# Kernel tuning notes

Hardware: AMD Instinct MI355X
Metric: run time of the kernel (lower is better)

Reference implementation:

```python
import jax, jax.numpy as jnp
import numpy as np

DIM = 256
QK_DIM = 256
NUM_HEADS = 8
N_WIN = 7
TOPK = 4
SCALE = QK_DIM ** (-0.5)


def setup_inputs() -> dict:
    key = jax.random.key(0)
    k1, k2, k3 = jax.random.split(key, 3)
    N, D, H, W, C = 2, 8, 56, 56, DIM
    x = jax.random.normal(k1, (N, D, H, W, C), dtype=jnp.float32)
    # QKVLinear: Linear(dim, qk_dim + qk_dim + dim)
    Wqkv = jax.random.normal(k2, (C, 2 * QK_DIM + DIM), dtype=jnp.float32) * 0.02
    bqkv = jnp.zeros((2 * QK_DIM + DIM,), dtype=jnp.float32)
    Wo = jax.random.normal(k3, (DIM, DIM), dtype=jnp.float32) * 0.02
    bo = jnp.zeros((DIM,), dtype=jnp.float32)
    return {"x": x, "Wqkv": Wqkv, "bqkv": bqkv, "Wo": Wo, "bo": bo}


def reference(x, Wqkv, bqkv, Wo, bo):
    N, D, H, W, C = x.shape
    j = i = N_WIN
    h, w = H // j, W // i
    p2, w2 = j * i, h * w
    n = N * D
    m = NUM_HEADS
    ch = QK_DIM // m   # qk head dim
    cv = DIM // m      # v head dim

    # n t (j h) (i w) c -> n t (j i) h w c
    xw = x.reshape(N, D, j, h, i, w, C).transpose(0, 1, 2, 4, 3, 5, 6)
    xw = xw.reshape(N, D, p2, h, w, C)

    # QKVLinear then split into q / kv
    qkv = xw @ Wqkv + bqkv                       # (N,D,p2,h,w,2qk+dim)
    q = qkv[..., :QK_DIM]                        # (N,D,p2,h,w,qk)
    kv = qkv[..., QK_DIM:]                       # (N,D,p2,h,w,qk+dim)

    # inter-frame shift: frame t uses kv of frame t+1; last frame keeps its own
    kv = jnp.concatenate([kv[:, 1:], kv[:, -1:]], axis=1)

    q = q.reshape(n, p2, h, w, QK_DIM)
    kv = kv.reshape(n, p2, h, w, QK_DIM + DIM)
    q_pix = q.reshape(n, p2, w2, QK_DIM)
    kv_pix = kv.reshape(n, p2, w2, QK_DIM + DIM)  # identity kv_down

    # window-level routing (diff_routing=False -> detached)
    q_win = jax.lax.stop_gradient(q.mean(axis=(2, 3)))                  # (n,p2,qk)
    k_win = jax.lax.stop_gradient(kv[..., :QK_DIM].mean(axis=(2, 3)))   # (n,p2,qk)
    attn_logit = jnp.einsum('npc,nqc->npq', q_win * SCALE, k_win)       # (n,p2,p2)
    topk_logit, r_idx = jax.lax.top_k(attn_logit, TOPK)                 # (n,p2,topk)
    r_weight = jax.nn.softmax(topk_logit, axis=-1)  # computed, unused (mul_weight='none')

    # gather kv of routed windows: (n,p2,topk,w2,qk+dim)
    kv_sel = jax.vmap(lambda kvp, idx: kvp[idx])(kv_pix, r_idx)

    k_sel = kv_sel[..., :QK_DIM].reshape(n, p2, TOPK * w2, m, ch)
    v_sel = kv_sel[..., QK_DIM:].reshape(n, p2, TOPK * w2, m, cv)
    qh = q_pix.reshape(n, p2, w2, m, ch)

    attn = jnp.einsum('npqmc,npkmc->npmqk', qh * SCALE, k_sel)  # (n,p2,m,w2,topk*w2)
    attn = jax.nn.softmax(attn, axis=-1)
    out = jnp.einsum('npmqk,npkmc->npqmc', attn, v_sel).reshape(n, p2, w2, C)

    # (n j i) (h w) c -> N D (j h) (i w) c
    out = out.reshape(N, D, j, i, h, w, C).transpose(0, 1, 2, 4, 3, 5, 6)
    out = out.reshape(N, D, H, W, C)
    out = out @ Wo + bo
    return out
```

## Files before the change

### kernel.cpp

```cpp
#include <hip/hip_runtime.h>
#include <hip/hip_bf16.h>
#include <math.h>

#define QSC 0.09016844f

typedef __attribute__((ext_vector_type(8))) short bf16x8;
typedef __attribute__((ext_vector_type(4))) float f32x4;

__device__ __forceinline__ ushort f2bf(float f) {
    unsigned u = __float_as_uint(f);
    return (ushort)((u + 0x7FFFu + ((u >> 16) & 1u)) >> 16);
}

__device__ __forceinline__ unsigned pk2bf(float a, float b) {
    __hip_bfloat162 h = __float22bfloat162_rn(make_float2(a, b));
    return *(unsigned*)&h;
}

__device__ __forceinline__ void gl_lds16(const ushort* g, ushort* l) {
    __builtin_amdgcn_global_load_lds(
        (const __attribute__((address_space(1))) unsigned int*)g,
        (__attribute__((address_space(3))) unsigned int*)l, 16, 0, 0);
}

__device__ __forceinline__ int swz(int row) { return (row ^ (row >> 2)) & 3; }

__device__ __forceinline__ int token_to_xrow(int t) {
    int nd  = t / 3136;
    int r   = t % 3136;
    int p   = r >> 6;
    int pix = r & 63;
    int j = p / 7, i = p % 7;
    int hh = pix >> 3, ww = pix & 7;
    return nd * 3136 + (j * 8 + hh) * 56 + (i * 8 + ww);
}

__global__ __launch_bounds__(256) void k_prep(const float* __restrict__ x,
                                              const float* __restrict__ Wqkv,
                                              const float* __restrict__ Wo,
                                              ushort* __restrict__ xg,
                                              float* __restrict__ xmean,
                                              ushort* __restrict__ Wqkvt,
                                              ushort* __restrict__ Wot) {
    int b = blockIdx.x;
    int tid = threadIdx.x;
    if (b >= 784) {
        int bb = b - 784;
        if (bb < 768) Wqkvt[bb * 256 + tid] = f2bf(Wqkv[(size_t)tid * 768 + bb]);
        else { int n = bb - 768; Wot[n * 256 + tid] = f2bf(Wo[(size_t)tid * 256 + n]); }
        return;
    }
    int nd = b / 49, p = b % 49;
    int j = p / 7, i = p % 7;
    const float* xb = x + ((size_t)nd * 3136 + (j * 8) * 56 + i * 8) * 256 + tid;
    ushort* xo = xg + (size_t)b * 64 * 256 + tid;
    float s = 0.f;
#pragma unroll 2
    for (int hh = 0; hh < 8; ++hh)
#pragma unroll
        for (int ww = 0; ww < 8; ++ww) {
            float v = xb[(size_t)(hh * 56 + ww) * 256];
            s += v;
            xo[(size_t)(hh * 8 + ww) * 256] = f2bf(v);
        }
    xmean[(size_t)b * 256 + tid] = s * (1.f / 64.f);
}

__global__ __launch_bounds__(256) void k_winproj(const float* __restrict__ xmean,
                                                 const float* __restrict__ Wqkv,
                                                 const float* __restrict__ bqkv,
                                                 float* __restrict__ qwin,
                                                 float* __restrict__ kwin) {
    __shared__ float As[16 * 68];
    __shared__ float Bs[16 * 64];
    const int tid = threadIdx.x;
    const int m0 = blockIdx.y * 64;
    const int n0 = blockIdx.x * 64;

    const int ar = tid >> 2;
    const int ak = (tid & 3) * 4;
    const int arow = (m0 + ar < 784) ? (m0 + ar) : 783;
    const float* aptr = xmean + (size_t)arow * 256 + ak;

    const int bk = tid >> 4;
    const int bn = (tid & 15) * 4;
    const float* bptr = Wqkv + (size_t)bk * 768 + n0 + bn;

    const int ty = tid >> 4, tx = tid & 15;
    float acc[4][4] = {};

    for (int kt = 0; kt < 256; kt += 16) {
        float4 av = *(const float4*)(aptr + kt);
        float4 bv = *(const float4*)(bptr + (size_t)kt * 768);
        __syncthreads();
        As[(ak + 0) * 68 + ar] = av.x;
        As[(ak + 1) * 68 + ar] = av.y;
        As[(ak + 2) * 68 + ar] = av.z;
        As[(ak + 3) * 68 + ar] = av.w;
        *(float4*)&Bs[bk * 64 + bn] = bv;
        __syncthreads();
#pragma unroll
        for (int kk = 0; kk < 16; ++kk) {
            float4 a4 = *(const float4*)&As[kk * 68 + ty * 4];
            float4 b4 = *(const float4*)&Bs[kk * 64 + tx * 4];
            float a[4] = {a4.x, a4.y, a4.z, a4.w};
            float b[4] = {b4.x, b4.y, b4.z, b4.w};
#pragma unroll
            for (int ii = 0; ii < 4; ++ii)
#pragma unroll
                for (int jj = 0; jj < 4; ++jj) acc[ii][jj] += a[ii] * b[jj];
        }
    }
#pragma unroll
    for (int ii = 0; ii < 4; ++ii) {
        int t = m0 + ty * 4 + ii;
        if (t >= 784) continue;
#pragma unroll
        for (int jj = 0; jj < 4; ++jj) {
            int col = n0 + tx * 4 + jj;
            float v = acc[ii][jj] + bqkv[col];
            if (col < 256) qwin[(size_t)t * 256 + col] = v;
            else           kwin[(size_t)t * 256 + (col - 256)] = v;
        }
    }
}

__global__ __launch_bounds__(256) void k_route(const float* __restrict__ qwin,
                                               const float* __restrict__ kwin,
                                               int* __restrict__ ridx) {
    const int b = blockIdx.x;
    const int nd = b / 49;
    const int ndkv = ((nd & 7) == 7) ? nd : nd + 1;
    const int tid = threadIdx.x;
    const int t = tid & 63, w = tid >> 6;
    __shared__ float qs[256];
    __shared__ float part[4][64];
    qs[tid] = qwin[b * 256 + tid];
    __syncthreads();
    float s = 0.f;
    if (t < 49) {
        const float* kr = kwin + ((size_t)ndkv * 49 + t) * 256 + w * 64;
#pragma unroll
        for (int c = 0; c < 64; c += 4) {
            float4 k4 = *(const float4*)(kr + c);
            float4 q4 = *(const float4*)&qs[w * 64 + c];
            s += q4.x * k4.x + q4.y * k4.y + q4.z * k4.z + q4.w * k4.w;
        }
    }
    part[w][t] = s;
    __syncthreads();
    if (tid < 64) {
        float logit = (t < 49) ? (part[0][t] + part[1][t] + part[2][t] + part[3][t])
                               : -INFINITY;
        for (int sel = 0; sel < 4; ++sel) {
            float v = logit;
            int ix = t;
            for (int off = 32; off > 0; off >>= 1) {
                float ov = __shfl_xor(v, off);
                int   oi = __shfl_xor(ix, off);
                if (ov > v || (ov == v && oi < ix)) { v = ov; ix = oi; }
            }
            if (t == 0) ridx[b * 4 + sel] = ix;
            if (t == ix) logit = -INFINITY;
        }
    }
}

__global__ __launch_bounds__(256) void k_gemm_qkv(const ushort* __restrict__ A,
                                                  const ushort* __restrict__ Bt,
                                                  const float* __restrict__ bqkv,
                                                  ushort* __restrict__ q,
                                                  ushort* __restrict__ kv) {
    __shared__ ushort As[2][128 * 32];
    __shared__ ushort Bs[2][128 * 32];
    const int tid = threadIdx.x;
    const int wv = tid >> 6, ln = tid & 63;
    const int lane15 = ln & 15, quad = ln >> 4;

    const int lin  = blockIdx.x + blockIdx.y * 6;
    const int work = (lin & 7) * 294 + (lin >> 3);
    const int n0 = (work % 6) * 128;
    const int m0 = (work / 6) * 128;

    const int row0 = tid >> 2, ck0 = tid & 3;
    const ushort* gA[2]; const ushort* gB[2];
    int lofs[2];
#pragma unroll
    for (int p = 0; p < 2; ++p) {
        int r = p * 64 + row0;
        int cks = ck0 ^ swz(r);
        gA[p] = A  + (size_t)(m0 + r) * 256 + cks * 8;
        gB[p] = Bt + (size_t)(n0 + r) * 256 + cks * 8;
        lofs[p] = (p * 256 + tid) * 8;
    }

    f32x4 acc[4][4];
#pragma unroll
    for (int i = 0; i < 4; ++i)
#pragma unroll
        for (int j = 0; j < 4; ++j) acc[i][j] = (f32x4){0.f, 0.f, 0.f, 0.f};

    const int mb = (wv >> 1) * 64, nb = (wv & 1) * 64;

#pragma unroll
    for (int p = 0; p < 2; ++p) {
        gl_lds16(gA[p], &As[0][lofs[p]]);
        gl_lds16(gB[p], &Bs[0][lofs[p]]);
    }
    asm volatile("s_waitcnt vmcnt(0)" ::: "memory");
    __builtin_amdgcn_s_barrier();

    int cur = 0;
#pragma unroll
    for (int kt = 0; kt < 8; ++kt) {
        if (kt < 7) {
#pragma unroll
            for (int p = 0; p < 2; ++p) {
                gl_lds16(gA[p] + (kt + 1) * 32, &As[cur ^ 1][lofs[p]]);
                gl_lds16(gB[p] + (kt + 1) * 32, &Bs[cur ^ 1][lofs[p]]);
            }
        }
        __builtin_amdgcn_sched_barrier(0);
        bf16x8 aF[4], bF[4];
#pragma unroll
        for (int mt = 0; mt < 4; ++mt) {
            int r = mb + mt * 16 + lane15;
            aF[mt] = *(const bf16x8*)&As[cur][r * 32 + (quad ^ swz(r)) * 8];
        }
#pragma unroll
        for (int nt = 0; nt < 4; ++nt) {
            int r = nb + nt * 16 + lane15;
            bF[nt] = *(const bf16x8*)&Bs[cur][r * 32 + (quad ^ swz(r)) * 8];
        }
#pragma unroll
        for (int mt = 0; mt < 4; ++mt)
#pragma unroll
            for (int nt = 0; nt < 4; ++nt)
                acc[mt][nt] = __builtin_amdgcn_mfma_f32_16x16x32_bf16(aF[mt], bF[nt], acc[mt][nt], 0, 0, 0);
        __builtin_amdgcn_sched_barrier(0);
        asm volatile("s_waitcnt vmcnt(0)" ::: "memory");
        __builtin_amdgcn_s_barrier();
        cur ^= 1;
    }

#pragma unroll
    for (int mt = 0; mt < 4; ++mt) {
#pragma unroll
        for (int nt = 0; nt < 4; ++nt) {
            int col = n0 + nb + nt * 16 + lane15;
            float bias = bqkv[col];
#pragma unroll
            for (int r = 0; r < 4; ++r) {
                int t = m0 + mb + mt * 16 + quad * 4 + r;
                float v = acc[mt][nt][r] + bias;
                if (col < 256) q[(size_t)t * 256 + col] = f2bf(v * QSC);
                else           kv[(size_t)t * 512 + (col - 256)] = f2bf(v);
            }
        }
    }
}

__global__ __launch_bounds__(256) void k_gemm_o(const ushort* __restrict__ A,
                                                const ushort* __restrict__ Bt,
                                                const float* __restrict__ bo,
                                                float* __restrict__ out) {
    __shared__ ushort As[2][128 * 32];
    __shared__ ushort Bs[2][128 * 32];
    const int tid = threadIdx.x;
    const int wv = tid >> 6, ln = tid & 63;
    const int lane15 = ln & 15, quad = ln >> 4;

    const int lin  = blockIdx.x + blockIdx.y * 2;
    const int work = (lin & 7) * 98 + (lin >> 3);
    const int n0 = (work % 2) * 128;
    const int m0 = (work / 2) * 128;

    const int row0 = tid >> 2, ck0 = tid & 3;
    const ushort* gA[2]; const ushort* gB[2];
    int lofs[2];
#pragma unroll
    for (int p = 0; p < 2; ++p) {
        int r = p * 64 + row0;
        int cks = ck0 ^ swz(r);
        gA[p] = A  + (size_t)(m0 + r) * 256 + cks * 8;
        gB[p] = Bt + (size_t)(n0 + r) * 256 + cks * 8;
        lofs[p] = (p * 256 + tid) * 8;
    }

    f32x4 acc[4][4];
#pragma unroll
    for (int i = 0; i < 4; ++i)
#pragma unroll
        for (int j = 0; j < 4; ++j) acc[i][j] = (f32x4){0.f, 0.f, 0.f, 0.f};

    const int mb = (wv >> 1) * 64, nb = (wv & 1) * 64;

#pragma unroll
    for (int p = 0; p < 2; ++p) {
        gl_lds16(gA[p], &As[0][lofs[p]]);
        gl_lds16(gB[p], &Bs[0][lofs[p]]);
    }
    asm volatile("s_waitcnt vmcnt(0)" ::: "memory");
    __builtin_amdgcn_s_barrier();

    int cur = 0;
#pragma unroll
    for (int kt = 0; kt < 8; ++kt) {
        if (kt < 7) {
#pragma unroll
            for (int p = 0; p < 2; ++p) {
                gl_lds16(gA[p] + (kt + 1) * 32, &As[cur ^ 1][lofs[p]]);
                gl_lds16(gB[p] + (kt + 1) * 32, &Bs[cur ^ 1][lofs[p]]);
            }
        }
        __builtin_amdgcn_sched_barrier(0);
        bf16x8 aF[4], bF[4];
#pragma unroll
        for (int mt = 0; mt < 4; ++mt) {
            int r = mb + mt * 16 + lane15;
            aF[mt] = *(const bf16x8*)&As[cur][r * 32 + (quad ^ swz(r)) * 8];
        }
#pragma unroll
        for (int nt = 0; nt < 4; ++nt) {
            int r = nb + nt * 16 + lane15;
            bF[nt] = *(const bf16x8*)&Bs[cur][r * 32 + (quad ^ swz(r)) * 8];
        }
#pragma unroll
        for (int mt = 0; mt < 4; ++mt)
#pragma unroll
            for (int nt = 0; nt < 4; ++nt)
                acc[mt][nt] = __builtin_amdgcn_mfma_f32_16x16x32_bf16(aF[mt], bF[nt], acc[mt][nt], 0, 0, 0);
        __builtin_amdgcn_sched_barrier(0);
        asm volatile("s_waitcnt vmcnt(0)" ::: "memory");
        __builtin_amdgcn_s_barrier();
        cur ^= 1;
    }

#pragma unroll
    for (int mt = 0; mt < 4; ++mt) {
#pragma unroll
        for (int nt = 0; nt < 4; ++nt) {
            int col = n0 + nb + nt * 16 + lane15;
            float bias = bo[col];
#pragma unroll
            for (int r = 0; r < 4; ++r) {
                int t = m0 + mb + mt * 16 + quad * 4 + r;
                int xr = token_to_xrow(t);
                out[(size_t)xr * 256 + col] = acc[mt][nt][r] + bias;
            }
        }
    }
}

__global__ __launch_bounds__(256, 3) void k_attn(ushort* qbuf,
                                                 const ushort* __restrict__ kvbuf,
                                                 const int* __restrict__ ridx) {
    const int lin  = blockIdx.x + (blockIdx.y + blockIdx.z * 49) * 8;
    const int work = (lin & 7) * 784 + (lin >> 3);
    const int h = work & 7;
    const int rest = work >> 3;
    const int p = rest % 49;
    const int nd = rest / 49;

    const int ndkv = ((nd & 7) == 7) ? nd : nd + 1;
    const int tid = threadIdx.x;
    const int wv = tid >> 6, ln = tid & 63;
    const int lane15 = ln & 15, quad = ln >> 4;

    __shared__ ushort Ks[256 * 40];
    __shared__ ushort Vt[32 * 264];
    __shared__ ushort Ps[64 * 72];

    const int rb = (nd * 49 + p) * 4;
    int wid[4];
#pragma unroll
    for (int i = 0; i < 4; ++i) wid[i] = ridx[rb + i];

    const size_t kvband = (size_t)ndkv * 49;

    {
        int pix = tid >> 2, ck = tid & 3;
#pragma unroll
        for (int i = 0; i < 4; ++i) {
            size_t trow = (kvband + wid[i]) * 64 + pix;
            bf16x8 v = *(const bf16x8*)(kvbuf + trow * 512 + h * 32 + ck * 8);
            *(bf16x8*)&Ks[(i * 64 + pix) * 40 + ck * 8] = v;
        }
    }
    {
        int key_l = (tid & 31) * 2;
        int ch0 = (tid >> 5) * 4;
#pragma unroll
        for (int i = 0; i < 4; ++i) {
            size_t trow = (kvband + wid[i]) * 64;
            const ushort* g0 = kvbuf + (trow + key_l) * 512 + 256 + h * 32 + ch0;
            const ushort* g1 = g0 + 512;
            ushort4 a = *(const ushort4*)g0;
            ushort4 b = *(const ushort4*)g1;
            int kg = i * 64 + key_l;
            *(unsigned*)&Vt[(ch0 + 0) * 264 + kg] = (unsigned)a.x | ((unsigned)b.x << 16);
            *(unsigned*)&Vt[(ch0 + 1) * 264 + kg] = (unsigned)a.y | ((unsigned)b.y << 16);
            *(unsigned*)&Vt[(ch0 + 2) * 264 + kg] = (unsigned)a.z | ((unsigned)b.z << 16);
            *(unsigned*)&Vt[(ch0 + 3) * 264 + kg] = (unsigned)a.w | ((unsigned)b.w << 16);
        }
    }

    const size_t qrow0 = (size_t)(nd * 49 + p) * 64;
    bf16x8 bQ = *(const bf16x8*)(qbuf + (qrow0 + wv * 16 + lane15) * 256 + h * 32 + quad * 8);

    __syncthreads();

    f32x4 st[16];
#pragma unroll
    for (int t = 0; t < 16; ++t) {
        bf16x8 aK = *(const bf16x8*)&Ks[(t * 16 + lane15) * 40 + quad * 8];
        st[t] = __builtin_amdgcn_mfma_f32_16x16x32_bf16(aK, bQ, (f32x4){0.f, 0.f, 0.f, 0.f}, 0, 0, 0);
    }

    float sum = 0.f;
#pragma unroll
    for (int t = 0; t < 16; ++t)
#pragma unroll
        for (int r = 0; r < 4; ++r) {
            float e = __builtin_amdgcn_exp2f(st[t][r]);
            st[t][r] = e;
            sum += e;
        }
    sum += __shfl_xor(sum, 16);
    sum += __shfl_xor(sum, 32);
    const float inv = 1.f / sum;

    f32x4 oacc[2] = {{0.f, 0.f, 0.f, 0.f}, {0.f, 0.f, 0.f, 0.f}};
    const int prow = (wv * 16 + lane15) * 72;
#pragma unroll
    for (int cc = 0; cc < 4; ++cc) {
#pragma unroll
        for (int tt = 0; tt < 4; ++tt) {
            int t = cc * 4 + tt;
            uint2 pk;
            pk.x = pk2bf(st[t][0], st[t][1]);
            pk.y = pk2bf(st[t][2], st[t][3]);
            *(uint2*)&Ps[prow + tt * 16 + quad * 4] = pk;
        }
#pragma unroll
        for (int kt = 0; kt < 2; ++kt) {
            bf16x8 aP = *(const bf16x8*)&Ps[prow + kt * 32 + quad * 8];
#pragma unroll
            for (int nt = 0; nt < 2; ++nt) {
                bf16x8 bV = *(const bf16x8*)&Vt[(nt * 16 + lane15) * 264 + cc * 64 + kt * 32 + quad * 8];
                oacc[nt] = __builtin_amdgcn_mfma_f32_16x16x32_bf16(aP, bV, oacc[nt], 0, 0, 0);
            }
        }
    }

#pragma unroll
    for (int nt = 0; nt < 2; ++nt)
#pragma unroll
        for (int r = 0; r < 4; ++r) {
            int row = wv * 16 + quad * 4 + r;
            qbuf[(qrow0 + row) * 256 + h * 32 + nt * 16 + lane15] = f2bf(oacc[nt][r] * inv);
        }
}

extern "C" void kernel_launch(void* const* d_in, const int* in_sizes, int n_in,
                              void* d_out, int out_size, void* d_ws, size_t ws_size,
                              hipStream_t stream) {
    const float* x    = (const float*)d_in[0];
    const float* Wqkv = (const float*)d_in[1];
    const float* bqkv = (const float*)d_in[2];
    const float* Wo   = (const float*)d_in[3];
    const float* bo   = (const float*)d_in[4];
    float* out = (float*)d_out;

    char* ws = (char*)d_ws;
    ushort* xg    = (ushort*)ws;                    ws += (size_t)50176 * 256 * 2;
    ushort* q     = (ushort*)ws;                    ws += (size_t)50176 * 256 * 2;
    ushort* kv    = (ushort*)ws;                    ws += (size_t)50176 * 512 * 2;
    ushort* Wqkvt = (ushort*)ws;                    ws += (size_t)768 * 256 * 2;
    ushort* Wot   = (ushort*)ws;                    ws += (size_t)256 * 256 * 2;
    float*  xmean = (float*)ws;                     ws += (size_t)784 * 256 * 4;
    float*  qwin  = (float*)ws;                     ws += (size_t)784 * 256 * 4;
    float*  kwin  = (float*)ws;                     ws += (size_t)784 * 256 * 4;
    int*    ridx  = (int*)ws;

    k_prep    <<<1808, 256, 0, stream>>>(x, Wqkv, Wo, xg, xmean, Wqkvt, Wot);
    k_winproj <<<dim3(8, 13), 256, 0, stream>>>(xmean, Wqkv, bqkv, qwin, kwin);
    k_route   <<<784, 256, 0, stream>>>(qwin, kwin, ridx);
    k_gemm_qkv<<<dim3(6, 392), 256, 0, stream>>>(xg, Wqkvt, bqkv, q, kv);
    k_attn    <<<dim3(8, 49, 16), 256, 0, stream>>>(q, kv, ridx);
    k_gemm_o  <<<dim3(2, 392), 256, 0, stream>>>(q, Wot, bo, out);
}
```

Measured before the change: 233.4 us.

## Keep GEMM B operand in registers and deepen A pipeline to four stages

Both GEMM kernels now load their whole 128-column weight slice (K=256) into registers once per block, and only the A tile is streamed through LDS with a 4-buffer, 3-ahead global_load_lds pipeline. The QKV GEMM also processes two M tiles per block to reuse those registers, halving its grid. The output GEMM replaces the per-element token remap with per-window base arithmetic. The attention kernel raises wave priority around its MFMA sections. This removes B tile LDS traffic and some barrier stalls, but adds register pressure, with launch bounds requesting 2 blocks per CU.

Result: slower. 313.4 us (+34.3%).

```diff
diff --git a/kernel.cpp b/kernel.cpp
--- a/kernel.cpp
+++ b/kernel.cpp
@@ -24,16 +24,6 @@
 }
 
 __device__ __forceinline__ int swz(int row) { return (row ^ (row >> 2)) & 3; }
-
-__device__ __forceinline__ int token_to_xrow(int t) {
-    int nd  = t / 3136;
-    int r   = t % 3136;
-    int p   = r >> 6;
-    int pix = r & 63;
-    int j = p / 7, i = p % 7;
-    int hh = pix >> 3, ww = pix & 7;
-    return nd * 3136 + (j * 8 + hh) * 56 + (i * 8 + ww);
-}
 
 __global__ __launch_bounds__(256) void k_prep(const float* __restrict__ x,
                                               const float* __restrict__ Wqkv,
@@ -166,32 +156,47 @@
     }
 }
 
-__global__ __launch_bounds__(256) void k_gemm_qkv(const ushort* __restrict__ A,
-                                                  const ushort* __restrict__ Bt,
-                                                  const float* __restrict__ bqkv,
-                                                  ushort* __restrict__ q,
-                                                  ushort* __restrict__ kv) {
-    __shared__ ushort As[2][128 * 32];
-    __shared__ ushort Bs[2][128 * 32];
+__global__ __launch_bounds__(256, 2) void k_gemm_qkv(const ushort* __restrict__ A,
+                                                     const ushort* __restrict__ Bt,
+                                                     const float* __restrict__ bqkv,
+                                                     ushort* __restrict__ q,
+                                                     ushort* __restrict__ kv) {
+    constexpr int NS = 16;
+    __shared__ ushort As[4][4096];
     const int tid = threadIdx.x;
     const int wv = tid >> 6, ln = tid & 63;
     const int lane15 = ln & 15, quad = ln >> 4;
 
-    const int lin  = blockIdx.x + blockIdx.y * 6;
-    const int work = (lin & 7) * 294 + (lin >> 3);
-    const int n0 = (work % 6) * 128;
-    const int m0 = (work / 6) * 128;
+    const int lin  = blockIdx.x;
+    const int work = (lin & 7) * 147 + (lin >> 3);
+    const int mg   = work / 6;
+    const int n0   = (work % 6) * 128;
 
     const int row0 = tid >> 2, ck0 = tid & 3;
-    const ushort* gA[2]; const ushort* gB[2];
-    int lofs[2];
+    const ushort* gA0[2];
 #pragma unroll
     for (int p = 0; p < 2; ++p) {
         int r = p * 64 + row0;
         int cks = ck0 ^ swz(r);
-        gA[p] = A  + (size_t)(m0 + r) * 256 + cks * 8;
-        gB[p] = Bt + (size_t)(n0 + r) * 256 + cks * 8;
-        lofs[p] = (p * 256 + tid) * 8;
+        gA0[p] = A + (size_t)(mg * 256 + r) * 256 + cks * 8;
+    }
+
+#pragma unroll
+    for (int s = 0; s < 3; ++s)
+#pragma unroll
+        for (int p = 0; p < 2; ++p)
+            gl_lds16(gA0[p] + (s & 7) * 32, &As[s & 3][p * 2048 + tid * 8]);
+
+    const int mb = (wv >> 1) * 64, nb = (wv & 1) * 64;
+
+    bf16x8 bF[8][4];
+    float bias[4];
+#pragma unroll
+    for (int nt = 0; nt < 4; ++nt) {
+        const ushort* bp = Bt + (size_t)(n0 + nb + nt * 16 + lane15) * 256 + quad * 8;
+#pragma unroll
+        for (int kt = 0; kt < 8; ++kt) bF[kt][nt] = *(const bf16x8*)(bp + kt * 32);
+        bias[nt] = bqkv[n0 + nb + nt * 16 + lane15];
     }
 
     f32x4 acc[4][4];
@@ -200,91 +205,92 @@
 #pragma unroll
         for (int j = 0; j < 4; ++j) acc[i][j] = (f32x4){0.f, 0.f, 0.f, 0.f};
 
-    const int mb = (wv >> 1) * 64, nb = (wv & 1) * 64;
-
-#pragma unroll
-    for (int p = 0; p < 2; ++p) {
-        gl_lds16(gA[p], &As[0][lofs[p]]);
-        gl_lds16(gB[p], &Bs[0][lofs[p]]);
-    }
-    asm volatile("s_waitcnt vmcnt(0)" ::: "memory");
-    __builtin_amdgcn_s_barrier();
-
-    int cur = 0;
-#pragma unroll
-    for (int kt = 0; kt < 8; ++kt) {
-        if (kt < 7) {
-#pragma unroll
-            for (int p = 0; p < 2; ++p) {
-                gl_lds16(gA[p] + (kt + 1) * 32, &As[cur ^ 1][lofs[p]]);
-                gl_lds16(gB[p] + (kt + 1) * 32, &Bs[cur ^ 1][lofs[p]]);
-            }
-        }
+#pragma unroll
+    for (int s = 0; s < NS; ++s) {
+        if (s <= NS - 3)      asm volatile("s_waitcnt vmcnt(4) lgkmcnt(0)" ::: "memory");
+        else if (s == NS - 2) asm volatile("s_waitcnt vmcnt(2) lgkmcnt(0)" ::: "memory");
+        else                  asm volatile("s_waitcnt vmcnt(0) lgkmcnt(0)" ::: "memory");
         __builtin_amdgcn_sched_barrier(0);
-        bf16x8 aF[4], bF[4];
+        __builtin_amdgcn_s_barrier();
+        if (s + 3 < NS) {
+            const int g = s + 3;
+#pragma unroll
+            for (int p = 0; p < 2; ++p)
+                gl_lds16(gA0[p] + ((g >> 3) * 32768 + (g & 7) * 32),
+                         &As[g & 3][p * 2048 + tid * 8]);
+        }
+        const ushort* buf = As[s & 3];
+        bf16x8 aF[4];
 #pragma unroll
         for (int mt = 0; mt < 4; ++mt) {
             int r = mb + mt * 16 + lane15;
-            aF[mt] = *(const bf16x8*)&As[cur][r * 32 + (quad ^ swz(r)) * 8];
-        }
-#pragma unroll
-        for (int nt = 0; nt < 4; ++nt) {
-            int r = nb + nt * 16 + lane15;
-            bF[nt] = *(const bf16x8*)&Bs[cur][r * 32 + (quad ^ swz(r)) * 8];
+            aF[mt] = *(const bf16x8*)&buf[r * 32 + (quad ^ swz(r)) * 8];
         }
 #pragma unroll
         for (int mt = 0; mt < 4; ++mt)
 #pragma unroll
             for (int nt = 0; nt < 4; ++nt)
-                acc[mt][nt] = __builtin_amdgcn_mfma_f32_16x16x32_bf16(aF[mt], bF[nt], acc[mt][nt], 0, 0, 0);
-        __builtin_amdgcn_sched_barrier(0);
-        asm volatile("s_waitcnt vmcnt(0)" ::: "memory");
-        __builtin_amdgcn_s_barrier();
-        cur ^= 1;
-    }
-
-#pragma unroll
-    for (int mt = 0; mt < 4; ++mt) {
-#pragma unroll
-        for (int nt = 0; nt < 4; ++nt) {
-            int col = n0 + nb + nt * 16 + lane15;
-            float bias = bqkv[col];
-#pragma unroll
-            for (int r = 0; r < 4; ++r) {
-                int t = m0 + mb + mt * 16 + quad * 4 + r;
-                float v = acc[mt][nt][r] + bias;
-                if (col < 256) q[(size_t)t * 256 + col] = f2bf(v * QSC);
-                else           kv[(size_t)t * 512 + (col - 256)] = f2bf(v);
-            }
-        }
-    }
-}
-
-__global__ __launch_bounds__(256) void k_gemm_o(const ushort* __restrict__ A,
-                                                const ushort* __restrict__ Bt,
-                                                const float* __restrict__ bo,
-                                                float* __restrict__ out) {
-    __shared__ ushort As[2][128 * 32];
-    __shared__ ushort Bs[2][128 * 32];
+                acc[mt][nt] = __builtin_amdgcn_mfma_f32_16x16x32_bf16(aF[mt], bF[s & 7][nt], acc[mt][nt], 0, 0, 0);
+        if ((s & 7) == 7) {
+            const int t0 = mg * 256 + (s >> 3) * 128 + mb;
+#pragma unroll
+            for (int mt = 0; mt < 4; ++mt)
+#pragma unroll
+                for (int nt = 0; nt < 4; ++nt) {
+                    int col = n0 + nb + nt * 16 + lane15;
+#pragma unroll
+                    for (int r = 0; r < 4; ++r) {
+                        int t = t0 + mt * 16 + quad * 4 + r;
+                        float v = acc[mt][nt][r] + bias[nt];
+                        if (col < 256) q[(size_t)t * 256 + col] = f2bf(v * QSC);
+                        else           kv[(size_t)t * 512 + (col - 256)] = f2bf(v);
+                        acc[mt][nt][r] = 0.f;
+                    }
+                }
+        }
+    }
+}
+
+__global__ __launch_bounds__(256, 2) void k_gemm_o(const ushort* __restrict__ A,
+                                                   const ushort* __restrict__ Bt,
+                                                   const float* __restrict__ bo,
+                                                   float* __restrict__ out) {
+    constexpr int NS = 8;
+    __shared__ ushort As[4][4096];
     const int tid = threadIdx.x;
     const int wv = tid >> 6, ln = tid & 63;
     const int lane15 = ln & 15, quad = ln >> 4;
 
-    const int lin  = blockIdx.x + blockIdx.y * 2;
-    const int work = (lin & 7) * 98 + (lin >> 3);
-    const int n0 = (work % 2) * 128;
-    const int m0 = (work / 2) * 128;
+    const int lin   = blockIdx.x;
+    const int work  = (lin & 7) * 98 + (lin >> 3);
+    const int mtile = work >> 1;
+    const int n0    = (work & 1) * 128;
 
     const int row0 = tid >> 2, ck0 = tid & 3;
-    const ushort* gA[2]; const ushort* gB[2];
-    int lofs[2];
+    const ushort* gA0[2];
 #pragma unroll
     for (int p = 0; p < 2; ++p) {
         int r = p * 64 + row0;
         int cks = ck0 ^ swz(r);
-        gA[p] = A  + (size_t)(m0 + r) * 256 + cks * 8;
-        gB[p] = Bt + (size_t)(n0 + r) * 256 + cks * 8;
-        lofs[p] = (p * 256 + tid) * 8;
+        gA0[p] = A + (size_t)(mtile * 128 + r) * 256 + cks * 8;
+    }
+
+#pragma unroll
+    for (int s = 0; s < 3; ++s)
+#pragma unroll
+        for (int p = 0; p < 2; ++p)
+            gl_lds16(gA0[p] + s * 32, &As[s][p * 2048 + tid * 8]);
+
+    const int mb = (wv >> 1) * 64, nb = (wv & 1) * 64;
+
+    bf16x8 bF[8][4];
+    float bias[4];
+#pragma unroll
+    for (int nt = 0; nt < 4; ++nt) {
+        const ushort* bp = Bt + (size_t)(n0 + nb + nt * 16 + lane15) * 256 + quad * 8;
+#pragma unroll
+        for (int kt = 0; kt < 8; ++kt) bF[kt][nt] = *(const bf16x8*)(bp + kt * 32);
+        bias[nt] = bo[n0 + nb + nt * 16 + lane15];
     }
 
     f32x4 acc[4][4];
@@ -293,63 +299,48 @@
 #pragma unroll
         for (int j = 0; j < 4; ++j) acc[i][j] = (f32x4){0.f, 0.f, 0.f, 0.f};
 
-    const int mb = (wv >> 1) * 64, nb = (wv & 1) * 64;
-
-#pragma unroll
-    for (int p = 0; p < 2; ++p) {
-        gl_lds16(gA[p], &As[0][lofs[p]]);
-        gl_lds16(gB[p], &Bs[0][lofs[p]]);
-    }
-    asm volatile("s_waitcnt vmcnt(0)" ::: "memory");
-    __builtin_amdgcn_s_barrier();
-
-    int cur = 0;
-#pragma unroll
-    for (int kt = 0; kt < 8; ++kt) {
-        if (kt < 7) {
-#pragma unroll
-            for (int p = 0; p < 2; ++p) {
-                gl_lds16(gA[p] + (kt + 1) * 32, &As[cur ^ 1][lofs[p]]);
-                gl_lds16(gB[p] + (kt + 1) * 32, &Bs[cur ^ 1][lofs[p]]);
-            }
-        }
+#pragma unroll
+    for (int s = 0; s < NS; ++s) {
+        if (s <= NS - 3)      asm volatile("s_waitcnt vmcnt(4) lgkmcnt(0)" ::: "memory");
+        else if (s == NS - 2) asm volatile("s_waitcnt vmcnt(2) lgkmcnt(0)" ::: "memory");
+        else                  asm volatile("s_waitcnt vmcnt(0) lgkmcnt(0)" ::: "memory");
         __builtin_amdgcn_sched_barrier(0);
-        bf16x8 aF[4], bF[4];
+        __builtin_amdgcn_s_barrier();
+        if (s + 3 < NS) {
+            const int g = s + 3;
+#pragma unroll
+            for (int p = 0; p < 2; ++p)
+                gl_lds16(gA0[p] + g * 32, &As[g & 3][p * 2048 + tid * 8]);
+        }
+        const ushort* buf = As[s & 3];
+        bf16x8 aF[4];
 #pragma unroll
         for (int mt = 0; mt < 4; ++mt) {
             int r = mb + mt * 16 + lane15;
-            aF[mt] = *(const bf16x8*)&As[cur][r * 32 + (quad ^ swz(r)) * 8];
-        }
-#pragma unroll
-        for (int nt = 0; nt < 4; ++nt) {
-            int r = nb + nt * 16 + lane15;
-            bF[nt] = *(const bf16x8*)&Bs[cur][r * 32 + (quad ^ swz(r)) * 8];
+            aF[mt] = *(const bf16x8*)&buf[r * 32 + (quad ^ swz(r)) * 8];
         }
 #pragma unroll
         for (int mt = 0; mt < 4; ++mt)
 #pragma unroll
             for (int nt = 0; nt < 4; ++nt)
-                acc[mt][nt] = __builtin_amdgcn_mfma_f32_16x16x32_bf16(aF[mt], bF[nt], acc[mt][nt], 0, 0, 0);
-        __builtin_amdgcn_sched_barrier(0);
-        asm volatile("s_waitcnt vmcnt(0)" ::: "memory");
-        __builtin_amdgcn_s_barrier();
-        cur ^= 1;
-    }
-
-#pragma unroll
-    for (int mt = 0; mt < 4; ++mt) {
+                acc[mt][nt] = __builtin_amdgcn_mfma_f32_16x16x32_bf16(aF[mt], bF[s & 7][nt], acc[mt][nt], 0, 0, 0);
+    }
+
+    const int w6 = (mtile * 128 + mb) >> 6;
+    const int ndw = w6 / 49, pw = w6 % 49;
+    const int wbase = ndw * 3136 + (pw / 7) * 8 * 56 + (pw % 7) * 8;
+#pragma unroll
+    for (int mt = 0; mt < 4; ++mt)
 #pragma unroll
         for (int nt = 0; nt < 4; ++nt) {
             int col = n0 + nb + nt * 16 + lane15;
-            float bias = bo[col];
 #pragma unroll
             for (int r = 0; r < 4; ++r) {
-                int t = m0 + mb + mt * 16 + quad * 4 + r;
-                int xr = token_to_xrow(t);
-                out[(size_t)xr * 256 + col] = acc[mt][nt][r] + bias;
+                int pix = mt * 16 + quad * 4 + r;
+                int xr = wbase + (pix >> 3) * 56 + (pix & 7);
+                out[(size_t)xr * 256 + col] = acc[mt][nt][r] + bias[nt];
             }
         }
-    }
 }
 
 __global__ __launch_bounds__(256, 3) void k_attn(ushort* qbuf,
@@ -411,11 +402,13 @@
     __syncthreads();
 
     f32x4 st[16];
+    __builtin_amdgcn_s_setprio(1);
 #pragma unroll
     for (int t = 0; t < 16; ++t) {
         bf16x8 aK = *(const bf16x8*)&Ks[(t * 16 + lane15) * 40 + quad * 8];
         st[t] = __builtin_amdgcn_mfma_f32_16x16x32_bf16(aK, bQ, (f32x4){0.f, 0.f, 0.f, 0.f}, 0, 0, 0);
     }
+    __builtin_amdgcn_s_setprio(0);
 
     float sum = 0.f;
 #pragma unroll
@@ -442,6 +435,7 @@
             pk.y = pk2bf(st[t][2], st[t][3]);
             *(uint2*)&Ps[prow + tt * 16 + quad * 4] = pk;
         }
+        __builtin_amdgcn_s_setprio(1);
 #pragma unroll
         for (int kt = 0; kt < 2; ++kt) {
             bf16x8 aP = *(const bf16x8*)&Ps[prow + kt * 32 + quad * 8];
@@ -451,6 +445,7 @@
                 oacc[nt] = __builtin_amdgcn_mfma_f32_16x16x32_bf16(aP, bV, oacc[nt], 0, 0, 0);
             }
         }
+        __builtin_amdgcn_s_setprio(0);
     }
 
 #pragma unroll
@@ -486,7 +481,7 @@
     k_prep    <<<1808, 256, 0, stream>>>(x, Wqkv, Wo, xg, xmean, Wqkvt, Wot);
     k_winproj <<<dim3(8, 13), 256, 0, stream>>>(xmean, Wqkv, bqkv, qwin, kwin);
     k_route   <<<784, 256, 0, stream>>>(qwin, kwin, ridx);
-    k_gemm_qkv<<<dim3(6, 392), 256, 0, stream>>>(xg, Wqkvt, bqkv, q, kv);
+    k_gemm_qkv<<<1176, 256, 0, stream>>>(xg, Wqkvt, bqkv, q, kv);
     k_attn    <<<dim3(8, 49, 16), 256, 0, stream>>>(q, kv, ridx);
-    k_gemm_o  <<<dim3(2, 392), 256, 0, stream>>>(q, Wot, bo, out);
-}
+    k_gemm_o  <<<784, 256, 0, stream>>>(q, Wot, bo, out);
+}
```

## Triple-buffer GEMM K-loop, simplify output scatter, and raise MFMA priority in attention

Applied to the files above, without the earlier changes.

Both GEMM kernels go from a double-buffered LDS pipeline to a three-stage ring that prefetches two K-tiles ahead. They now wait with vmcnt(4) instead of draining every load, which keeps one tile in flight during compute. The output GEMM replaces the per-element token-to-pixel division with a per-wave window base plus a cheap offset, and launches on a 1D grid. The attention kernel wraps its MFMA sections in s_setprio to favor matrix issue. The extra stage raises LDS use per block, which may lower occupancy.

Result: no change. 231.4 us (-0.8%).

```diff
diff --git a/kernel.cpp b/kernel.cpp
--- a/kernel.cpp
+++ b/kernel.cpp
@@ -24,16 +24,6 @@
 }
 
 __device__ __forceinline__ int swz(int row) { return (row ^ (row >> 2)) & 3; }
-
-__device__ __forceinline__ int token_to_xrow(int t) {
-    int nd  = t / 3136;
-    int r   = t % 3136;
-    int p   = r >> 6;
-    int pix = r & 63;
-    int j = p / 7, i = p % 7;
-    int hh = pix >> 3, ww = pix & 7;
-    return nd * 3136 + (j * 8 + hh) * 56 + (i * 8 + ww);
-}
 
 __global__ __launch_bounds__(256) void k_prep(const float* __restrict__ x,
                                               const float* __restrict__ Wqkv,
@@ -171,8 +161,8 @@
                                                   const float* __restrict__ bqkv,
                                                   ushort* __restrict__ q,
                                                   ushort* __restrict__ kv) {
-    __shared__ ushort As[2][128 * 32];
-    __shared__ ushort Bs[2][128 * 32];
+    __shared__ ushort As[3][4096];
+    __shared__ ushort Bs[3][4096];
     const int tid = threadIdx.x;
     const int wv = tid >> 6, ln = tid & 63;
     const int lane15 = ln & 15, quad = ln >> 4;
@@ -203,34 +193,38 @@
     const int mb = (wv >> 1) * 64, nb = (wv & 1) * 64;
 
 #pragma unroll
-    for (int p = 0; p < 2; ++p) {
-        gl_lds16(gA[p], &As[0][lofs[p]]);
-        gl_lds16(gB[p], &Bs[0][lofs[p]]);
-    }
-    asm volatile("s_waitcnt vmcnt(0)" ::: "memory");
+    for (int s = 0; s < 2; ++s)
+#pragma unroll
+        for (int p = 0; p < 2; ++p) {
+            gl_lds16(gA[p] + s * 32, &As[s][lofs[p]]);
+            gl_lds16(gB[p] + s * 32, &Bs[s][lofs[p]]);
+        }
+    asm volatile("s_waitcnt vmcnt(4)" ::: "memory");
     __builtin_amdgcn_s_barrier();
 
-    int cur = 0;
 #pragma unroll
     for (int kt = 0; kt < 8; ++kt) {
-        if (kt < 7) {
+        if (kt < 6) {
+            const int g = kt + 2;
+            const int sl = g % 3;
 #pragma unroll
             for (int p = 0; p < 2; ++p) {
-                gl_lds16(gA[p] + (kt + 1) * 32, &As[cur ^ 1][lofs[p]]);
-                gl_lds16(gB[p] + (kt + 1) * 32, &Bs[cur ^ 1][lofs[p]]);
+                gl_lds16(gA[p] + g * 32, &As[sl][lofs[p]]);
+                gl_lds16(gB[p] + g * 32, &Bs[sl][lofs[p]]);
             }
         }
         __builtin_amdgcn_sched_barrier(0);
+        const int sl = kt % 3;
         bf16x8 aF[4], bF[4];
 #pragma unroll
         for (int mt = 0; mt < 4; ++mt) {
             int r = mb + mt * 16 + lane15;
-            aF[mt] = *(const bf16x8*)&As[cur][r * 32 + (quad ^ swz(r)) * 8];
+            aF[mt] = *(const bf16x8*)&As[sl][r * 32 + (quad ^ swz(r)) * 8];
         }
 #pragma unroll
         for (int nt = 0; nt < 4; ++nt) {
             int r = nb + nt * 16 + lane15;
-            bF[nt] = *(const bf16x8*)&Bs[cur][r * 32 + (quad ^ swz(r)) * 8];
+            bF[nt] = *(const bf16x8*)&Bs[sl][r * 32 + (quad ^ swz(r)) * 8];
         }
 #pragma unroll
         for (int mt = 0; mt < 4; ++mt)
@@ -238,9 +232,9 @@
             for (int nt = 0; nt < 4; ++nt)
                 acc[mt][nt] = __builtin_amdgcn_mfma_f32_16x16x32_bf16(aF[mt], bF[nt], acc[mt][nt], 0, 0, 0);
         __builtin_amdgcn_sched_barrier(0);
-        asm volatile("s_waitcnt vmcnt(0)" ::: "memory");
-        __builtin_amdgcn_s_barrier();
-        cur ^= 1;
+        if (kt < 6)      asm volatile("s_waitcnt vmcnt(4) lgkmcnt(0)" ::: "memory");
+        else if (kt == 6) asm volatile("s_waitcnt vmcnt(0) lgkmcnt(0)" ::: "memory");
+        if (kt < 7) __builtin_amdgcn_s_barrier();
     }
 
 #pragma unroll
@@ -264,13 +258,13 @@
                                                 const ushort* __restrict__ Bt,
                                                 const float* __restrict__ bo,
                                                 float* __restrict__ out) {
-    __shared__ ushort As[2][128 * 32];
-    __shared__ ushort Bs[2][128 * 32];
+    __shared__ ushort As[3][4096];
+    __shared__ ushort Bs[3][4096];
     const int tid = threadIdx.x;
     const int wv = tid >> 6, ln = tid & 63;
     const int lane15 = ln & 15, quad = ln >> 4;
 
-    const int lin  = blockIdx.x + blockIdx.y * 2;
+    const int lin  = blockIdx.x;
     const int work = (lin & 7) * 98 + (lin >> 3);
     const int n0 = (work % 2) * 128;
     const int m0 = (work / 2) * 128;
@@ -296,34 +290,38 @@
     const int mb = (wv >> 1) * 64, nb = (wv & 1) * 64;
 
 #pragma unroll
-    for (int p = 0; p < 2; ++p) {
-        gl_lds16(gA[p], &As[0][lofs[p]]);
-        gl_lds16(gB[p], &Bs[0][lofs[p]]);
-    }
-    asm volatile("s_waitcnt vmcnt(0)" ::: "memory");
+    for (int s = 0; s < 2; ++s)
+#pragma unroll
+        for (int p = 0; p < 2; ++p) {
+            gl_lds16(gA[p] + s * 32, &As[s][lofs[p]]);
+            gl_lds16(gB[p] + s * 32, &Bs[s][lofs[p]]);
+        }
+    asm volatile("s_waitcnt vmcnt(4)" ::: "memory");
     __builtin_amdgcn_s_barrier();
 
-    int cur = 0;
 #pragma unroll
     for (int kt = 0; kt < 8; ++kt) {
-        if (kt < 7) {
+        if (kt < 6) {
+            const int g = kt + 2;
+            const int sl = g % 3;
 #pragma unroll
             for (int p = 0; p < 2; ++p) {
-                gl_lds16(gA[p] + (kt + 1) * 32, &As[cur ^ 1][lofs[p]]);
-                gl_lds16(gB[p] + (kt + 1) * 32, &Bs[cur ^ 1][lofs[p]]);
+                gl_lds16(gA[p] + g * 32, &As[sl][lofs[p]]);
+                gl_lds16(gB[p] + g * 32, &Bs[sl][lofs[p]]);
             }
         }
         __builtin_amdgcn_sched_barrier(0);
+        const int sl = kt % 3;
         bf16x8 aF[4], bF[4];
 #pragma unroll
         for (int mt = 0; mt < 4; ++mt) {
             int r = mb + mt * 16 + lane15;
-            aF[mt] = *(const bf16x8*)&As[cur][r * 32 + (quad ^ swz(r)) * 8];
+            aF[mt] = *(const bf16x8*)&As[sl][r * 32 + (quad ^ swz(r)) * 8];
         }
 #pragma unroll
         for (int nt = 0; nt < 4; ++nt) {
             int r = nb + nt * 16 + lane15;
-            bF[nt] = *(const bf16x8*)&Bs[cur][r * 32 + (quad ^ swz(r)) * 8];
+            bF[nt] = *(const bf16x8*)&Bs[sl][r * 32 + (quad ^ swz(r)) * 8];
         }
 #pragma unroll
         for (int mt = 0; mt < 4; ++mt)
@@ -331,25 +329,27 @@
             for (int nt = 0; nt < 4; ++nt)
                 acc[mt][nt] = __builtin_amdgcn_mfma_f32_16x16x32_bf16(aF[mt], bF[nt], acc[mt][nt], 0, 0, 0);
         __builtin_amdgcn_sched_barrier(0);
-        asm volatile("s_waitcnt vmcnt(0)" ::: "memory");
-        __builtin_amdgcn_s_barrier();
-        cur ^= 1;
-    }
-
-#pragma unroll
-    for (int mt = 0; mt < 4; ++mt) {
+        if (kt < 6)      asm volatile("s_waitcnt vmcnt(4) lgkmcnt(0)" ::: "memory");
+        else if (kt == 6) asm volatile("s_waitcnt vmcnt(0) lgkmcnt(0)" ::: "memory");
+        if (kt < 7) __builtin_amdgcn_s_barrier();
+    }
+
+    const int w6 = (m0 + mb) >> 6;
+    const int ndw = w6 / 49, pw = w6 % 49;
+    const int wbase = ndw * 3136 + (pw / 7) * 8 * 56 + (pw % 7) * 8;
+#pragma unroll
+    for (int mt = 0; mt < 4; ++mt)
 #pragma unroll
         for (int nt = 0; nt < 4; ++nt) {
             int col = n0 + nb + nt * 16 + lane15;
             float bias = bo[col];
 #pragma unroll
             for (int r = 0; r < 4; ++r) {
-                int t = m0 + mb + mt * 16 + quad * 4 + r;
-                int xr = token_to_xrow(t);
+                int pix = mt * 16 + quad * 4 + r;
+                int xr = wbase + (pix >> 3) * 56 + (pix & 7);
                 out[(size_t)xr * 256 + col] = acc[mt][nt][r] + bias;
             }
         }
-    }
 }
 
 __global__ __launch_bounds__(256, 3) void k_attn(ushort* qbuf,
@@ -411,11 +411,13 @@
     __syncthreads();
 
     f32x4 st[16];
+    __builtin_amdgcn_s_setprio(1);
 #pragma unroll
     for (int t = 0; t < 16; ++t) {
         bf16x8 aK = *(const bf16x8*)&Ks[(t * 16 + lane15) * 40 + quad * 8];
         st[t] = __builtin_amdgcn_mfma_f32_16x16x32_bf16(aK, bQ, (f32x4){0.f, 0.f, 0.f, 0.f}, 0, 0, 0);
     }
+    __builtin_amdgcn_s_setprio(0);
 
     float sum = 0.f;
 #pragma unroll
@@ -442,6 +444,7 @@
             pk.y = pk2bf(st[t][2], st[t][3]);
             *(uint2*)&Ps[prow + tt * 16 + quad * 4] = pk;
         }
+        __builtin_amdgcn_s_setprio(1);
 #pragma unroll
         for (int kt = 0; kt < 2; ++kt) {
             bf16x8 aP = *(const bf16x8*)&Ps[prow + kt * 32 + quad * 8];
@@ -451,6 +454,7 @@
                 oacc[nt] = __builtin_amdgcn_mfma_f32_16x16x32_bf16(aP, bV, oacc[nt], 0, 0, 0);
             }
         }
+        __builtin_amdgcn_s_setprio(0);
     }
 
 #pragma unroll
@@ -488,5 +492,5 @@
     k_route   <<<784, 256, 0, stream>>>(qwin, kwin, ridx);
     k_gemm_qkv<<<dim3(6, 392), 256, 0, stream>>>(xg, Wqkvt, bqkv, q, kv);
     k_attn    <<<dim3(8, 49, 16), 256, 0, stream>>>(q, kv, ridx);
-    k_gemm_o  <<<dim3(2, 392), 256, 0, stream>>>(q, Wot, bo, out);
-}
+    k_gemm_o  <<<784, 256, 0, stream>>>(q, Wot, bo, out);
+}
```
